# Kernel tuning notes

Hardware: AMD Instinct MI355X
Metric: run time of the kernel (lower is better)

The kernel has to match this reference:

```python
import jax, jax.numpy as jnp
import numpy as np

H, W, C, E = 6, 40, 512, 128  # hardcoded in module


def setup_inputs() -> dict:
    key = jax.random.key(0)
    ks = jax.random.split(key, 9)
    nB = 512
    inp = {
        "prev_hidden": jax.random.normal(ks[0], (nB, C), jnp.float32),
        "conv_feats": jax.random.normal(ks[1], (nB, C, H, W), jnp.float32),
        "conv_feats_origin": jax.random.normal(ks[2], (nB, C, H, W), jnp.float32),
        "cur_embeddings": jax.random.normal(ks[3], (nB, E), jnp.float32),
        # params
        "score_w": jax.random.normal(ks[4], (C,), jnp.float32) * (1.0 / np.sqrt(C)),
        "w_ih": jax.random.normal(ks[5], (3 * C, C + E), jnp.float32) * (1.0 / np.sqrt(C)),
        "w_hh": jax.random.normal(ks[6], (3 * C, C), jnp.float32) * (1.0 / np.sqrt(C)),
        "b_ih": jax.random.normal(ks[7], (3 * C,), jnp.float32) * 0.01,
        "b_hh": jax.random.normal(ks[8], (3 * C,), jnp.float32) * 0.01,
    }
    return inp


def gru_cell(x, h, w_ih, w_hh, b_ih, b_hh):
    # PyTorch GRUCell semantics
    gi = x @ w_ih.T + b_ih            # [B, 3C]
    gh = h @ w_hh.T + b_hh            # [B, 3C]
    i_r, i_z, i_n = jnp.split(gi, 3, axis=1)
    h_r, h_z, h_n = jnp.split(gh, 3, axis=1)
    r = jax.nn.sigmoid(i_r + h_r)
    z = jax.nn.sigmoid(i_z + h_z)
    n = jnp.tanh(i_n + r * h_n)
    return (1.0 - z) * n + z * h


def reference(prev_hidden, conv_feats, conv_feats_origin, cur_embeddings,
              score_w, w_ih, w_hh, b_ih, b_hh):
    nB = prev_hidden.shape[0]
    cf = conv_feats.reshape(nB, C, H * W)          # [B, C, HW]
    cfo = conv_feats_origin.reshape(nB, C, H * W)  # [B, C, HW]
    # additive attention score: tanh(feat + h) . score_w
    e = jnp.tanh(cf + prev_hidden[:, :, None])      # [B, C, HW]
    emition = jnp.einsum('bch,c->bh', e, score_w)   # [B, HW]
    alpha = jax.nn.softmax(emition, axis=1)         # softmax over HW positions
    context = jnp.einsum('bch,bh->bc', cfo, alpha)  # [B, C]
    x = jnp.concatenate([context, cur_embeddings], axis=1)  # [B, C+E]
    cur_hidden = gru_cell(x, prev_hidden, w_ih, w_hh, b_ih, b_hh)
    return cur_hidden, alpha.T  # alpha returned as [HW, B] like the original
```

## Files before the change

### kernel.cpp

```cpp
#include <hip/hip_runtime.h>
#include <hip/hip_bf16.h>

#define B   512
#define C   512
#define HW  240
#define E   128
#define XD  640
#define G3  1536

#define N4_WIH 245760
#define N4_WHH 196608
#define N4_H    65536

typedef short  s8v  __attribute__((ext_vector_type(8)));
typedef float  f4v  __attribute__((ext_vector_type(4)));

__device__ __forceinline__ float fast_tanh(float x) {
    float ex = __expf(2.0f * x);
    return (ex - 1.0f) * __builtin_amdgcn_rcpf(ex + 1.0f);
}
__device__ __forceinline__ float fast_sigmoid(float x) {
    return __builtin_amdgcn_rcpf(1.0f + __expf(-x));
}
__device__ __forceinline__ unsigned short f2bf(float x) {
    return __builtin_bit_cast(unsigned short, __float2bfloat16(x));
}

__global__ __launch_bounds__(256) void emition_kernel(
    const float* __restrict__ prev_hidden,
    const float* __restrict__ conv_feats,
    const float* __restrict__ score_w,
    float* __restrict__ partials)
{
    const int b = blockIdx.x;
    const int chunk = blockIdx.y;
    const int c0 = chunk * 64;
    const int t = threadIdx.x;

    __shared__ float ph_s[64], sw_s[64];
    __shared__ float4 red[4 * 60];

    if (t < 64) {
        ph_s[t] = prev_hidden[b * C + c0 + t];
        sw_s[t] = score_w[c0 + t];
    }
    __syncthreads();

    if (t < 240) {
        const int cs = t / 60;
        const int i  = t % 60;
        const float4* base =
            (const float4*)(conv_feats + ((size_t)(b * C + c0 + cs * 16)) * HW) + i;
        float4 acc = {0.f, 0.f, 0.f, 0.f};
        #pragma unroll
        for (int j = 0; j < 16; ++j) {
            float4 v = base[j * (HW / 4)];
            float ph = ph_s[cs * 16 + j];
            float sw = sw_s[cs * 16 + j];
            acc.x += fast_tanh(v.x + ph) * sw;
            acc.y += fast_tanh(v.y + ph) * sw;
            acc.z += fast_tanh(v.z + ph) * sw;
            acc.w += fast_tanh(v.w + ph) * sw;
        }
        red[cs * 60 + i] = acc;
    }
    __syncthreads();

    if (t < 60) {
        float4 a = red[t], b4 = red[60 + t], c4 = red[120 + t], d4 = red[180 + t];
        float4 s;
        s.x = a.x + b4.x + c4.x + d4.x;
        s.y = a.y + b4.y + c4.y + d4.y;
        s.z = a.z + b4.z + c4.z + d4.z;
        s.w = a.w + b4.w + c4.w + d4.w;
        ((float4*)(partials + ((size_t)b * 8 + chunk) * HW))[t] = s;
    }
}

__global__ __launch_bounds__(256) void softmax_kernel(
    const float* __restrict__ partials,
    const float* __restrict__ cur_emb,
    float* __restrict__ alpha_f32,
    float* __restrict__ alpha_out,
    unsigned short* __restrict__ x_bf16)
{
    const int b = blockIdx.x, t = threadIdx.x;
    const int lane = t & 63, w = t >> 6;
    __shared__ float red[4];

    float e = -1e30f;
    if (t < HW) {
        const float* p = partials + (size_t)b * 8 * HW + t;
        float s0 = 0.f;
        #pragma unroll
        for (int k = 0; k < 8; ++k) s0 += p[k * HW];
        e = s0;
    }
    float m = e;
    #pragma unroll
    for (int off = 32; off >= 1; off >>= 1) m = fmaxf(m, __shfl_xor(m, off));
    if (lane == 0) red[w] = m;
    __syncthreads();
    m = fmaxf(fmaxf(red[0], red[1]), fmaxf(red[2], red[3]));

    float p = (t < HW) ? __expf(e - m) : 0.f;
    float s = p;
    #pragma unroll
    for (int off = 32; off >= 1; off >>= 1) s += __shfl_xor(s, off);
    __syncthreads();
    if (lane == 0) red[w] = s;
    __syncthreads();
    s = red[0] + red[1] + red[2] + red[3];
    float inv = __builtin_amdgcn_rcpf(s);

    if (t < HW) {
        float a = p * inv;
        alpha_f32[b * HW + t] = a;
        alpha_out[(size_t)t * B + b] = a;
    }
    if (t < E) x_bf16[(size_t)b * XD + C + t] = f2bf(cur_emb[b * E + t]);
}

__global__ __launch_bounds__(256) void context_kernel(
    const float* __restrict__ cfo,
    const float* __restrict__ alpha_f32,
    unsigned short* __restrict__ x_bf16)
{
    const int b = blockIdx.x, chunk = blockIdx.y, t = threadIdx.x;
    const int lane = t & 63, w = t >> 6;
    __shared__ float4 af4[60];
    if (t < 60) af4[t] = ((const float4*)(alpha_f32 + b * HW))[t];
    __syncthreads();

    const int r = chunk * 64 + w * 16 + (lane >> 2);
    const int q = lane & 3;
    const float4* row = (const float4*)(cfo + ((size_t)(b * C + r)) * HW);

    float acc = 0.f;
    #pragma unroll
    for (int k = 0; k < 15; ++k) {
        float4 v = row[q + 4 * k];
        float4 a = af4[q + 4 * k];
        acc += v.x * a.x + v.y * a.y + v.z * a.z + v.w * a.w;
    }
    acc += __shfl_xor(acc, 1);
    acc += __shfl_xor(acc, 2);
    if (q == 0) x_bf16[(size_t)b * XD + r] = f2bf(acc);
}

__global__ void cvt_all_kernel(const float4* __restrict__ wih,
                               const float4* __restrict__ whh,
                               const float4* __restrict__ h,
                               ushort4* __restrict__ wih_o,
                               ushort4* __restrict__ whh_o,
                               ushort4* __restrict__ h_o)
{
    int i = blockIdx.x * blockDim.x + threadIdx.x;
    const float4* src; ushort4* dst; int j;
    if (i < N4_WIH)                { src = wih; dst = wih_o; j = i; }
    else if (i < N4_WIH + N4_WHH)  { src = whh; dst = whh_o; j = i - N4_WIH; }
    else if (i < N4_WIH + N4_WHH + N4_H) { src = h; dst = h_o; j = i - N4_WIH - N4_WHH; }
    else return;
    float4 v = src[j];
    ushort4 o;
    o.x = f2bf(v.x); o.y = f2bf(v.y); o.z = f2bf(v.z); o.w = f2bf(v.w);
    dst[j] = o;
}

__global__ __launch_bounds__(256) void gemm_kernel(
    const unsigned short* __restrict__ x,
    const unsigned short* __restrict__ hprev,
    const unsigned short* __restrict__ wih,
    const unsigned short* __restrict__ whh,
    const float* __restrict__ b_ih, const float* __restrict__ b_hh,
    float* __restrict__ gi, float* __restrict__ gh)
{
    const int z = blockIdx.z;
    const unsigned short* Amat = z ? hprev : x;
    const unsigned short* Wmat = z ? whh : wih;
    const float* bias = z ? b_hh : b_ih;
    float* out = z ? gh : gi;
    const int K = z ? C : XD;

    const int b0 = blockIdx.x * 64;
    const int j0 = blockIdx.y * 64;

    __shared__ alignas(16) unsigned short As[64][72];
    __shared__ alignas(16) unsigned short Ws[64][72];

    const int t = threadIdx.x, lane = t & 63, w = t >> 6;
    const int wm = w & 1, wn = w >> 1;
    const int r = t >> 2, kq = t & 3;
    const int q = lane >> 4, mm = lane & 15;

    f4v z4 = {0.f, 0.f, 0.f, 0.f};
    f4v acc[2][2] = {{z4, z4}, {z4, z4}};

    for (int k0 = 0; k0 < K; k0 += 64) {
        const unsigned short* ga = &Amat[(size_t)(b0 + r) * K + k0 + kq * 8];
        const unsigned short* gw = &Wmat[(size_t)(j0 + r) * K + k0 + kq * 8];
        s8v a_lo = *(const s8v*)ga;
        s8v a_hi = *(const s8v*)(ga + 32);
        s8v w_lo = *(const s8v*)gw;
        s8v w_hi = *(const s8v*)(gw + 32);
        __syncthreads();
        *(s8v*)&As[r][kq * 8]      = a_lo;
        *(s8v*)&As[r][kq * 8 + 32] = a_hi;
        *(s8v*)&Ws[r][kq * 8]      = w_lo;
        *(s8v*)&Ws[r][kq * 8 + 32] = w_hi;
        __syncthreads();

        #pragma unroll
        for (int kk = 0; kk < 2; ++kk) {
            s8v a0 = *(const s8v*)&As[wm * 32 + mm][kk * 32 + q * 8];
            s8v a1 = *(const s8v*)&As[wm * 32 + 16 + mm][kk * 32 + q * 8];
            s8v w0 = *(const s8v*)&Ws[wn * 32 + mm][kk * 32 + q * 8];
            s8v w1 = *(const s8v*)&Ws[wn * 32 + 16 + mm][kk * 32 + q * 8];
            acc[0][0] = __builtin_amdgcn_mfma_f32_16x16x32_bf16(a0, w0, acc[0][0], 0, 0, 0);
            acc[0][1] = __builtin_amdgcn_mfma_f32_16x16x32_bf16(a0, w1, acc[0][1], 0, 0, 0);
            acc[1][0] = __builtin_amdgcn_mfma_f32_16x16x32_bf16(a1, w0, acc[1][0], 0, 0, 0);
            acc[1][1] = __builtin_amdgcn_mfma_f32_16x16x32_bf16(a1, w1, acc[1][1], 0, 0, 0);
        }
    }

    #pragma unroll
    for (int mi = 0; mi < 2; ++mi)
        #pragma unroll
        for (int ni = 0; ni < 2; ++ni) {
            int jj = j0 + wn * 32 + ni * 16 + mm;
            float bv = bias[jj];
            #pragma unroll
            for (int rg = 0; rg < 4; ++rg) {
                int bi = b0 + wm * 32 + mi * 16 + q * 4 + rg;
                out[(size_t)bi * G3 + jj] = acc[mi][ni][rg] + bv;
            }
        }
}

__global__ void gates_kernel(const float* __restrict__ gi,
                             const float* __restrict__ gh,
                             const float* __restrict__ hprev,
                             float* __restrict__ out)
{
    int idx = blockIdx.x * blockDim.x + threadIdx.x;
    if (idx >= B * C) return;
    int b = idx >> 9;
    int c = idx & 511;
    const float* gib = gi + (size_t)b * G3;
    const float* ghb = gh + (size_t)b * G3;
    float r  = fast_sigmoid(gib[c] + ghb[c]);
    float zz = fast_sigmoid(gib[c + C] + ghb[c + C]);
    float n  = fast_tanh(gib[c + 2 * C] + r * ghb[c + 2 * C]);
    out[idx] = (1.f - zz) * n + zz * hprev[idx];
}

extern "C" void kernel_launch(void* const* d_in, const int* in_sizes, int n_in,
                              void* d_out, int out_size, void* d_ws, size_t ws_size,
                              hipStream_t stream)
{
    const float* prev_hidden = (const float*)d_in[0];
    const float* conv_feats  = (const float*)d_in[1];
    const float* cfo         = (const float*)d_in[2];
    const float* emb         = (const float*)d_in[3];
    const float* score_w     = (const float*)d_in[4];
    const float* w_ih        = (const float*)d_in[5];
    const float* w_hh        = (const float*)d_in[6];
    const float* b_ih        = (const float*)d_in[7];
    const float* b_hh        = (const float*)d_in[8];

    float* out       = (float*)d_out;
    float* alpha_out = out + B * C;

    char* ws = (char*)d_ws;
    float* partials          = (float*)(ws);
    float* gi                = (float*)(ws);
    float* gh                = (float*)(ws + 3932160);
    float* alpha_f32         = (float*)(ws + 7077888);
    unsigned short* x_bf16   = (unsigned short*)(ws + 7569408);
    unsigned short* h_bf16   = (unsigned short*)(ws + 8224768);
    unsigned short* wih_bf   = (unsigned short*)(ws + 8749056);
    unsigned short* whh_bf   = (unsigned short*)(ws + 10715136);

    {
        int n4 = N4_WIH + N4_WHH + N4_H;
        cvt_all_kernel<<<(n4 + 255) / 256, 256, 0, stream>>>(
            (const float4*)w_ih, (const float4*)w_hh, (const float4*)prev_hidden,
            (ushort4*)wih_bf, (ushort4*)whh_bf, (ushort4*)h_bf16);
    }

    emition_kernel<<<dim3(B, 8), 256, 0, stream>>>(prev_hidden, conv_feats, score_w, partials);
    softmax_kernel<<<B, 256, 0, stream>>>(partials, emb, alpha_f32, alpha_out, x_bf16);
    context_kernel<<<dim3(B, 8), 256, 0, stream>>>(cfo, alpha_f32, x_bf16);

    gemm_kernel<<<dim3(8, 24, 2), 256, 0, stream>>>(x_bf16, h_bf16, wih_bf, whh_bf,
                                                    b_ih, b_hh, gi, gh);

    gates_kernel<<<(B * C + 255) / 256, 256, 0, stream>>>(gi, gh, prev_hidden, out);
}
```

Measured before the change: 520.6 us.

## Fuse softmax into context kernel and convert weights to bf16 inside GEMM

```diff
diff --git a/kernel.cpp b/kernel.cpp
--- a/kernel.cpp
+++ b/kernel.cpp
@@ -8,10 +8,6 @@
 #define XD  640
 #define G3  1536
 
-#define N4_WIH 245760
-#define N4_WHH 196608
-#define N4_H    65536
-
 typedef short  s8v  __attribute__((ext_vector_type(8)));
 typedef float  f4v  __attribute__((ext_vector_type(4)));
 
@@ -24,6 +20,14 @@
 }
 __device__ __forceinline__ unsigned short f2bf(float x) {
     return __builtin_bit_cast(unsigned short, __float2bfloat16(x));
+}
+__device__ __forceinline__ s8v pack8(float4 a, float4 b) {
+    s8v o;
+    o[0] = (short)f2bf(a.x); o[1] = (short)f2bf(a.y);
+    o[2] = (short)f2bf(a.z); o[3] = (short)f2bf(a.w);
+    o[4] = (short)f2bf(b.x); o[5] = (short)f2bf(b.y);
+    o[6] = (short)f2bf(b.z); o[7] = (short)f2bf(b.w);
+    return o;
 }
 
 __global__ __launch_bounds__(256) void emition_kernel(
@@ -77,15 +81,16 @@
     }
 }
 
-__global__ __launch_bounds__(256) void softmax_kernel(
+__global__ __launch_bounds__(256) void ctx_softmax_kernel(
     const float* __restrict__ partials,
+    const float* __restrict__ cfo,
     const float* __restrict__ cur_emb,
-    float* __restrict__ alpha_f32,
     float* __restrict__ alpha_out,
     unsigned short* __restrict__ x_bf16)
 {
-    const int b = blockIdx.x, t = threadIdx.x;
+    const int b = blockIdx.x, chunk = blockIdx.y, t = threadIdx.x;
     const int lane = t & 63, w = t >> 6;
+    __shared__ float4 af4[60];
     __shared__ float red[4];
 
     float e = -1e30f;
@@ -112,24 +117,13 @@
     __syncthreads();
     s = red[0] + red[1] + red[2] + red[3];
     float inv = __builtin_amdgcn_rcpf(s);
-
-    if (t < HW) {
-        float a = p * inv;
-        alpha_f32[b * HW + t] = a;
-        alpha_out[(size_t)t * B + b] = a;
-    }
-    if (t < E) x_bf16[(size_t)b * XD + C + t] = f2bf(cur_emb[b * E + t]);
-}
-
-__global__ __launch_bounds__(256) void context_kernel(
-    const float* __restrict__ cfo,
-    const float* __restrict__ alpha_f32,
-    unsigned short* __restrict__ x_bf16)
-{
-    const int b = blockIdx.x, chunk = blockIdx.y, t = threadIdx.x;
-    const int lane = t & 63, w = t >> 6;
-    __shared__ float4 af4[60];
-    if (t < 60) af4[t] = ((const float4*)(alpha_f32 + b * HW))[t];
+    float a = p * inv;
+
+    if (t < HW) ((float*)af4)[t] = a;
+    if (chunk == 0) {
+        if (t < HW) alpha_out[(size_t)t * B + b] = a;
+        if (t < E)  x_bf16[(size_t)b * XD + C + t] = f2bf(cur_emb[b * E + t]);
+    }
     __syncthreads();
 
     const int r = chunk * 64 + w * 16 + (lane >> 2);
@@ -140,44 +134,24 @@
     #pragma unroll
     for (int k = 0; k < 15; ++k) {
         float4 v = row[q + 4 * k];
-        float4 a = af4[q + 4 * k];
-        acc += v.x * a.x + v.y * a.y + v.z * a.z + v.w * a.w;
+        float4 av = af4[q + 4 * k];
+        acc += v.x * av.x + v.y * av.y + v.z * av.z + v.w * av.w;
     }
     acc += __shfl_xor(acc, 1);
     acc += __shfl_xor(acc, 2);
     if (q == 0) x_bf16[(size_t)b * XD + r] = f2bf(acc);
 }
 
-__global__ void cvt_all_kernel(const float4* __restrict__ wih,
-                               const float4* __restrict__ whh,
-                               const float4* __restrict__ h,
-                               ushort4* __restrict__ wih_o,
-                               ushort4* __restrict__ whh_o,
-                               ushort4* __restrict__ h_o)
-{
-    int i = blockIdx.x * blockDim.x + threadIdx.x;
-    const float4* src; ushort4* dst; int j;
-    if (i < N4_WIH)                { src = wih; dst = wih_o; j = i; }
-    else if (i < N4_WIH + N4_WHH)  { src = whh; dst = whh_o; j = i - N4_WIH; }
-    else if (i < N4_WIH + N4_WHH + N4_H) { src = h; dst = h_o; j = i - N4_WIH - N4_WHH; }
-    else return;
-    float4 v = src[j];
-    ushort4 o;
-    o.x = f2bf(v.x); o.y = f2bf(v.y); o.z = f2bf(v.z); o.w = f2bf(v.w);
-    dst[j] = o;
-}
-
 __global__ __launch_bounds__(256) void gemm_kernel(
     const unsigned short* __restrict__ x,
-    const unsigned short* __restrict__ hprev,
-    const unsigned short* __restrict__ wih,
-    const unsigned short* __restrict__ whh,
+    const float* __restrict__ hprev,
+    const float* __restrict__ wih,
+    const float* __restrict__ whh,
     const float* __restrict__ b_ih, const float* __restrict__ b_hh,
     float* __restrict__ gi, float* __restrict__ gh)
 {
     const int z = blockIdx.z;
-    const unsigned short* Amat = z ? hprev : x;
-    const unsigned short* Wmat = z ? whh : wih;
+    const float* Wmat = z ? whh : wih;
     const float* bias = z ? b_hh : b_ih;
     float* out = z ? gh : gi;
     const int K = z ? C : XD;
@@ -190,36 +164,44 @@
 
     const int t = threadIdx.x, lane = t & 63, w = t >> 6;
     const int wm = w & 1, wn = w >> 1;
-    const int r = t >> 2, kq = t & 3;
+    const int r = t >> 2, col0 = (t & 3) * 16;
     const int q = lane >> 4, mm = lane & 15;
 
     f4v z4 = {0.f, 0.f, 0.f, 0.f};
     f4v acc[2][2] = {{z4, z4}, {z4, z4}};
 
     for (int k0 = 0; k0 < K; k0 += 64) {
-        const unsigned short* ga = &Amat[(size_t)(b0 + r) * K + k0 + kq * 8];
-        const unsigned short* gw = &Wmat[(size_t)(j0 + r) * K + k0 + kq * 8];
-        s8v a_lo = *(const s8v*)ga;
-        s8v a_hi = *(const s8v*)(ga + 32);
-        s8v w_lo = *(const s8v*)gw;
-        s8v w_hi = *(const s8v*)(gw + 32);
+        s8v a0, a1, w0, w1;
+        if (z) {
+            const float4* pa = (const float4*)&hprev[(size_t)(b0 + r) * C + k0 + col0];
+            float4 f0 = pa[0], f1 = pa[1], f2 = pa[2], f3 = pa[3];
+            a0 = pack8(f0, f1); a1 = pack8(f2, f3);
+        } else {
+            const unsigned short* pa = &x[(size_t)(b0 + r) * XD + k0 + col0];
+            a0 = *(const s8v*)pa; a1 = *(const s8v*)(pa + 8);
+        }
+        {
+            const float4* pw = (const float4*)&Wmat[(size_t)(j0 + r) * K + k0 + col0];
+            float4 f0 = pw[0], f1 = pw[1], f2 = pw[2], f3 = pw[3];
+            w0 = pack8(f0, f1); w1 = pack8(f2, f3);
+        }
         __syncthreads();
-        *(s8v*)&As[r][kq * 8]      = a_lo;
-        *(s8v*)&As[r][kq * 8 + 32] = a_hi;
-        *(s8v*)&Ws[r][kq * 8]      = w_lo;
-        *(s8v*)&Ws[r][kq * 8 + 32] = w_hi;
+        *(s8v*)&As[r][col0]     = a0;
+        *(s8v*)&As[r][col0 + 8] = a1;
+        *(s8v*)&Ws[r][col0]     = w0;
+        *(s8v*)&Ws[r][col0 + 8] = w1;
         __syncthreads();
 
         #pragma unroll
         for (int kk = 0; kk < 2; ++kk) {
-            s8v a0 = *(const s8v*)&As[wm * 32 + mm][kk * 32 + q * 8];
-            s8v a1 = *(const s8v*)&As[wm * 32 + 16 + mm][kk * 32 + q * 8];
-            s8v w0 = *(const s8v*)&Ws[wn * 32 + mm][kk * 32 + q * 8];
-            s8v w1 = *(const s8v*)&Ws[wn * 32 + 16 + mm][kk * 32 + q * 8];
-            acc[0][0] = __builtin_amdgcn_mfma_f32_16x16x32_bf16(a0, w0, acc[0][0], 0, 0, 0);
-            acc[0][1] = __builtin_amdgcn_mfma_f32_16x16x32_bf16(a0, w1, acc[0][1], 0, 0, 0);
-            acc[1][0] = __builtin_amdgcn_mfma_f32_16x16x32_bf16(a1, w0, acc[1][0], 0, 0, 0);
-            acc[1][1] = __builtin_amdgcn_mfma_f32_16x16x32_bf16(a1, w1, acc[1][1], 0, 0, 0);
+            s8v av0 = *(const s8v*)&As[wm * 32 + mm][kk * 32 + q * 8];
+            s8v av1 = *(const s8v*)&As[wm * 32 + 16 + mm][kk * 32 + q * 8];
+            s8v wv0 = *(const s8v*)&Ws[wn * 32 + mm][kk * 32 + q * 8];
+            s8v wv1 = *(const s8v*)&Ws[wn * 32 + 16 + mm][kk * 32 + q * 8];
+            acc[0][0] = __builtin_amdgcn_mfma_f32_16x16x32_bf16(av0, wv0, acc[0][0], 0, 0, 0);
+            acc[0][1] = __builtin_amdgcn_mfma_f32_16x16x32_bf16(av0, wv1, acc[0][1], 0, 0, 0);
+            acc[1][0] = __builtin_amdgcn_mfma_f32_16x16x32_bf16(av1, wv0, acc[1][0], 0, 0, 0);
+            acc[1][1] = __builtin_amdgcn_mfma_f32_16x16x32_bf16(av1, wv1, acc[1][1], 0, 0, 0);
         }
     }
 
@@ -275,25 +257,11 @@
     float* partials          = (float*)(ws);
     float* gi                = (float*)(ws);
     float* gh                = (float*)(ws + 3932160);
-    float* alpha_f32         = (float*)(ws + 7077888);
-    unsigned short* x_bf16   = (unsigned short*)(ws + 7569408);
-    unsigned short* h_bf16   = (unsigned short*)(ws + 8224768);
-    unsigned short* wih_bf   = (unsigned short*)(ws + 8749056);
-    unsigned short* whh_bf   = (unsigned short*)(ws + 10715136);
-
-    {
-        int n4 = N4_WIH + N4_WHH + N4_H;
-        cvt_all_kernel<<<(n4 + 255) / 256, 256, 0, stream>>>(
-            (const float4*)w_ih, (const float4*)w_hh, (const float4*)prev_hidden,
-            (ushort4*)wih_bf, (ushort4*)whh_bf, (ushort4*)h_bf16);
-    }
+    unsigned short* x_bf16   = (unsigned short*)(ws + 7077888);
 
     emition_kernel<<<dim3(B, 8), 256, 0, stream>>>(prev_hidden, conv_feats, score_w, partials);
-    softmax_kernel<<<B, 256, 0, stream>>>(partials, emb, alpha_f32, alpha_out, x_bf16);
-    context_kernel<<<dim3(B, 8), 256, 0, stream>>>(cfo, alpha_f32, x_bf16);
-
-    gemm_kernel<<<dim3(8, 24, 2), 256, 0, stream>>>(x_bf16, h_bf16, wih_bf, whh_bf,
+    ctx_softmax_kernel<<<dim3(B, 8), 256, 0, stream>>>(partials, cfo, emb, alpha_out, x_bf16);
+    gemm_kernel<<<dim3(8, 24, 2), 256, 0, stream>>>(x_bf16, prev_hidden, w_ih, w_hh,
                                                     b_ih, b_hh, gi, gh);
-
     gates_kernel<<<(B * C + 255) / 256, 256, 0, stream>>>(gi, gh, prev_hidden, out);
 }
```

Result: no change. 517.9 us (-0.5%).
